# Kernel tuning notes

Hardware: AMD Instinct MI355X
Metric: run time of the kernel (lower is better)

Reference implementation:

```python
import jax, jax.numpy as jnp
import numpy as np

B, S, D, H = 8, 2048, 1024, 128  # batch, seq (== CONTEXT_WINDOW), embed dim, headspace


def setup_inputs() -> dict:
    key = jax.random.key(0)
    ks = jax.random.split(key, 7)
    scale = 1.0 / np.sqrt(D)
    return {
        "x": jax.random.normal(ks[0], (B, S, D), dtype=jnp.float32),
        "Wq": jax.random.normal(ks[1], (D, H), dtype=jnp.float32) * scale,
        "bq": jax.random.normal(ks[2], (H,), dtype=jnp.float32) * 0.01,
        "Wk": jax.random.normal(ks[3], (D, H), dtype=jnp.float32) * scale,
        "bk": jax.random.normal(ks[4], (H,), dtype=jnp.float32) * 0.01,
        "Wv": jax.random.normal(ks[5], (D, H), dtype=jnp.float32) * scale,
        "bv": jax.random.normal(ks[6], (H,), dtype=jnp.float32) * 0.01,
    }


def reference(x, Wq, bq, Wk, bk, Wv, bv):
    # x: [B, S, D]
    embedlen = x.shape[-1]
    q = x @ Wq + bq  # [B, S, H]
    k = x @ Wk + bk  # [B, S, H]
    v = x @ Wv + bv  # [B, S, H]
    # NOTE: original code MULTIPLIES by sqrt(embedlen) (embedlen = full embed dim) --
    # faithful reproduction of the source, not the standard 1/sqrt(head_dim).
    scale = jnp.sqrt(jnp.asarray(embedlen, dtype=x.dtype))
    scores = jnp.einsum("bsh,bth->bst", q, k) * scale  # [B, S, S]
    seqlen = x.shape[1]
    causal = jnp.tril(jnp.ones((seqlen, seqlen), dtype=bool))
    scores = jnp.where(causal, scores, -jnp.inf)
    attn = jax.nn.softmax(scores, axis=-1)
    return jnp.einsum("bst,bth->bsh", attn, v)  # [B, S, H]
```

## Files before the change

### kernel.cpp

```cpp
#include <hip/hip_runtime.h>
#include <math.h>

#define SEQ 2048
#define DIM 1024
#define HD  128
#define NB  8
#define M_TOT (NB * SEQ)

typedef __attribute__((ext_vector_type(8))) short   short8;
typedef __attribute__((ext_vector_type(4))) float   floatx4;

__device__ __forceinline__ unsigned short f2bf(float f) {
    unsigned u = __builtin_bit_cast(unsigned, f);
    u += 0x7FFFu + ((u >> 16) & 1u);
    return (unsigned short)(u >> 16);
}
__device__ __forceinline__ float bf2f(unsigned short h) {
    unsigned u = ((unsigned)h) << 16;
    return __builtin_bit_cast(float, u);
}
__device__ __forceinline__ void async16(const void* g, void* l) {
    __builtin_amdgcn_global_load_lds(
        (const __attribute__((address_space(1))) unsigned int*)g,
        (__attribute__((address_space(3))) unsigned int*)l, 16, 0, 0);
}

#define MFMA16(a, b, c) __builtin_amdgcn_mfma_f32_16x16x32_bf16((a), (b), (c), 0, 0, 0)

__global__ __launch_bounds__(256) void wt_prep(
    const float* __restrict__ Wq, const float* __restrict__ Wk, const float* __restrict__ Wv,
    unsigned short* __restrict__ Wth, unsigned short* __restrict__ Wtl)
{
    int idx = blockIdx.x * 256 + threadIdx.x;
    int k   = idx & 1023;
    int n   = (idx >> 10) & 127;
    int mat = idx >> 17;
    const float* W = (mat == 0) ? Wq : (mat == 1) ? Wk : Wv;
    float v = W[k * HD + n];
    unsigned short hi = f2bf(v);
    Wth[idx] = hi;
    Wtl[idx] = f2bf(v - bf2f(hi));
}

__global__ __launch_bounds__(256) void qkv_gemm(
    const float* __restrict__ x,
    const unsigned short* __restrict__ Wth, const unsigned short* __restrict__ Wtl,
    const float* __restrict__ bq, const float* __restrict__ bk, const float* __restrict__ bv,
    unsigned short* __restrict__ Qh, unsigned short* __restrict__ Ql,
    unsigned short* __restrict__ Kh, unsigned short* __restrict__ Kl,
    unsigned short* __restrict__ Vt)
{
    __shared__ short lds[48 * 512];

    const int t    = threadIdx.x;
    const int lane = t & 63;
    const int w    = t >> 6;
    const int lrow = lane & 15;
    const int quad = lane >> 4;

    const int mat = blockIdx.x;
    const int R0  = blockIdx.y * 64;
    const int mh  = w & 1;
    const int nh  = w >> 1;

    floatx4 acc[2][4];
    const floatx4 zf = {0.f, 0.f, 0.f, 0.f};
    #pragma unroll
    for (int i = 0; i < 2; ++i)
        #pragma unroll
        for (int j = 0; j < 4; ++j) acc[i][j] = zf;

    const size_t wmat = (size_t)mat * (HD * DIM);

    auto stage = [&](int k0, int q) {
        const float* xp = x + (size_t)(R0 + w * 16 + lrow) * DIM + k0 + quad * 8;
        float4 xa = *(const float4*)xp;
        float4 xb = *(const float4*)(xp + 4);
        float xv[8] = {xa.x, xa.y, xa.z, xa.w, xb.x, xb.y, xb.z, xb.w};
        short8 hv, lv;
        #pragma unroll
        for (int i = 0; i < 8; ++i) {
            unsigned short h = f2bf(xv[i]);
            hv[i] = (short)h;
            lv[i] = (short)f2bf(xv[i] - bf2f(h));
        }
        *(short8*)&lds[(q * 24 + w * 2 + 0) * 512 + lane * 8] = hv;
        *(short8*)&lds[(q * 24 + w * 2 + 1) * 512 + lane * 8] = lv;
        #pragma unroll
        for (int i = 0; i < 4; ++i) {
            int id = w * 4 + i;
            int p = id & 1, nf = id >> 1;
            const unsigned short* src = (p ? Wtl : Wth) + wmat
                + (size_t)(nf * 16 + lrow) * DIM + k0 + quad * 8;
            async16(src, &lds[(q * 24 + 8 + id) * 512 + lane * 8]);
        }
    };

    stage(0, 0);
    for (int it = 0; it < 32; ++it) {
        __syncthreads();
        if (it < 31) stage((it + 1) * 32, (it + 1) & 1);
        const int q = it & 1;

        short8 a[2][2];
        #pragma unroll
        for (int mi = 0; mi < 2; ++mi)
            #pragma unroll
            for (int p = 0; p < 2; ++p)
                a[mi][p] = *(short8*)&lds[(q * 24 + (2 * mh + mi) * 2 + p) * 512 + lane * 8];

        #pragma unroll
        for (int ni = 0; ni < 4; ++ni) {
            int nf = nh * 4 + ni;
            short8 bh = *(short8*)&lds[(q * 24 + 8 + nf * 2 + 0) * 512 + lane * 8];
            #pragma unroll
            for (int mi = 0; mi < 2; ++mi)
                acc[mi][ni] = MFMA16(a[mi][0], bh, acc[mi][ni]);
            if (mat < 2) {
                short8 bl = *(short8*)&lds[(q * 24 + 8 + nf * 2 + 1) * 512 + lane * 8];
                #pragma unroll
                for (int mi = 0; mi < 2; ++mi) {
                    acc[mi][ni] = MFMA16(a[mi][0], bl, acc[mi][ni]);
                    acc[mi][ni] = MFMA16(a[mi][1], bh, acc[mi][ni]);
                }
            }
        }
    }

    const float* bias = (mat == 0) ? bq : (mat == 1) ? bk : bv;
    #pragma unroll
    for (int ni = 0; ni < 4; ++ni) {
        int col = (nh * 4 + ni) * 16 + lrow;
        float bval = bias[col];
        #pragma unroll
        for (int mi = 0; mi < 2; ++mi) {
            #pragma unroll
            for (int reg = 0; reg < 4; ++reg) {
                int gm = R0 + (2 * mh + mi) * 16 + quad * 4 + reg;
                float v = acc[mi][ni][reg] + bval;
                if (mat == 0) {
                    v *= 32.0f;
                    unsigned short h = f2bf(v);
                    Qh[(size_t)gm * HD + col] = h;
                    Ql[(size_t)gm * HD + col] = f2bf(v - bf2f(h));
                } else if (mat == 1) {
                    unsigned short h = f2bf(v);
                    Kh[(size_t)gm * HD + col] = h;
                    Kl[(size_t)gm * HD + col] = f2bf(v - bf2f(h));
                } else {
                    int b = gm >> 11, s = gm & 2047;
                    Vt[((size_t)b * HD + col) * SEQ + s] = f2bf(v);
                }
            }
        }
    }
}

__global__ __launch_bounds__(256) void flash_attn(
    const unsigned short* __restrict__ Qh, const unsigned short* __restrict__ Ql,
    const unsigned short* __restrict__ Kh, const unsigned short* __restrict__ Kl,
    const unsigned short* __restrict__ Vt, float* __restrict__ out,
    float* __restrict__ Opart, float* __restrict__ ML, int split)
{
    __shared__ short lds[52 * 512];

    const int t    = threadIdx.x;
    const int lane = t & 63;
    const int w    = t >> 6;
    const int lrow = lane & 15;
    const int quad = lane >> 4;

    const int idx = blockIdx.x;
    const int b   = idx & 7;
    const int h   = split ? ((idx >> 3) & 1) : 0;
    const int s   = split ? (63 - (idx >> 4)) : (63 - (idx >> 3));
    const int T   = (s + 2) >> 1;
    const int Th  = (T + 1) >> 1;
    const int t0  = split ? (h ? Th : 0) : 0;
    const int t1  = split ? (h ? T : Th) : T;

    if (split && t0 >= t1) {
        float* op = Opart + (size_t)idx * 4096;
        for (int i = t; i < 4096; i += 256) op[i] = 0.0f;
        if (t < 32) { ML[(idx * 32 + t) * 2] = -1e30f; ML[(idx * 32 + t) * 2 + 1] = 0.0f; }
        return;
    }

    const int mh = w & 1;
    const int kh = w >> 1;
    const int R  = s * 32 + mh * 16;

    const size_t kbase = (size_t)b * SEQ * HD;
    const size_t vbase = (size_t)b * HD * SEQ;

    short8 qf[4][2];
    #pragma unroll
    for (int kc = 0; kc < 4; ++kc) {
        size_t off = kbase + (size_t)(R + lrow) * HD + kc * 32 + quad * 8;
        qf[kc][0] = *(const short8*)(Qh + off);
        qf[kc][1] = *(const short8*)(Ql + off);
    }

    const floatx4 zf = {0.f, 0.f, 0.f, 0.f};
    floatx4 accO[8];
    #pragma unroll
    for (int i = 0; i < 8; ++i) accO[i] = zf;
    float m_[4] = {-1e30f, -1e30f, -1e30f, -1e30f};
    float l_[4] = {0.f, 0.f, 0.f, 0.f};

    for (int it = t0; it < t1; ++it) {
        const int j0 = it * 64;
        __syncthreads();
        #pragma unroll
        for (int i = 0; i < 12; ++i) {
            int id = w * 12 + i;
            const unsigned short* src;
            if (id < 32) {
                int nt = id >> 3, kc = (id >> 1) & 3, p = id & 1;
                src = (p ? Kl : Kh) + kbase
                    + (size_t)(j0 + nt * 16 + lrow) * HD + kc * 32 + quad * 8;
            } else {
                int v = id - 32, df = v >> 1, kc = v & 1;
                src = Vt + vbase + (size_t)(df * 16 + lrow) * SEQ
                    + j0 + kc * 32 + quad * 8;
            }
            async16(src, &lds[id * 512 + lane * 8]);
        }
        __syncthreads();

        floatx4 S[2] = {zf, zf};
        #pragma unroll
        for (int ntl = 0; ntl < 2; ++ntl) {
            int nt = kh * 2 + ntl;
            #pragma unroll
            for (int kc = 0; kc < 4; ++kc) {
                short8 khf = *(short8*)&lds[(nt * 8 + kc * 2 + 0) * 512 + lane * 8];
                short8 klf = *(short8*)&lds[(nt * 8 + kc * 2 + 1) * 512 + lane * 8];
                S[ntl] = MFMA16(qf[kc][0], khf, S[ntl]);
                S[ntl] = MFMA16(qf[kc][0], klf, S[ntl]);
                S[ntl] = MFMA16(qf[kc][1], khf, S[ntl]);
            }
        }
        if (j0 + kh * 32 + 31 > R) {
            #pragma unroll
            for (int ntl = 0; ntl < 2; ++ntl) {
                int key = j0 + (kh * 2 + ntl) * 16 + lrow;
                #pragma unroll
                for (int reg = 0; reg < 4; ++reg) {
                    if (key > R + quad * 4 + reg) S[ntl][reg] = -INFINITY;
                }
            }
        }
        float alpha[4];
        #pragma unroll
        for (int reg = 0; reg < 4; ++reg) {
            float mx = fmaxf(S[0][reg], S[1][reg]);
            #pragma unroll
            for (int hh = 1; hh < 16; hh <<= 1) mx = fmaxf(mx, __shfl_xor(mx, hh));
            float mnew = fmaxf(fmaxf(m_[reg], mx), -1e30f);
            alpha[reg] = __expf(m_[reg] - mnew);
            m_[reg] = mnew;
            float p0 = __expf(S[0][reg] - mnew);
            float p1 = __expf(S[1][reg] - mnew);
            S[0][reg] = p0; S[1][reg] = p1;
            float ls = p0 + p1;
            #pragma unroll
            for (int hh = 1; hh < 16; hh <<= 1) ls += __shfl_xor(ls, hh);
            l_[reg] = l_[reg] * alpha[reg] + ls;
        }
        #pragma unroll
        for (int i = 0; i < 8; ++i)
            #pragma unroll
            for (int reg = 0; reg < 4; ++reg) accO[i][reg] *= alpha[reg];

        #pragma unroll
        for (int ntl = 0; ntl < 2; ++ntl) {
            #pragma unroll
            for (int reg = 0; reg < 4; ++reg) {
                int kloc = ntl * 16 + lrow;
                int jj = kloc & 7, q2 = (kloc >> 3) & 3;
                int lane2 = (quad * 4 + reg) + (q2 << 4);
                lds[(48 + w) * 512 + lane2 * 8 + jj] = (short)f2bf(S[ntl][reg]);
            }
        }
        short8 pf = *(short8*)&lds[(48 + w) * 512 + lane * 8];
        #pragma unroll
        for (int df = 0; df < 8; ++df) {
            short8 vf = *(short8*)&lds[(32 + df * 2 + kh) * 512 + lane * 8];
            accO[df] = MFMA16(pf, vf, accO[df]);
        }
    }

    __syncthreads();
    float* fl   = (float*)lds;
    float* Obuf = fl;
    float* mlb  = fl + 4096;
    if (lrow == 0) {
        #pragma unroll
        for (int reg = 0; reg < 4; ++reg) {
            int row = quad * 4 + reg;
            mlb[((kh * 2 + mh) * 16 + row) * 2 + 0] = m_[reg];
            mlb[((kh * 2 + mh) * 16 + row) * 2 + 1] = l_[reg];
        }
    }
    __syncthreads();
    float myw[4], Mrow[4], Drow[4];
    #pragma unroll
    for (int reg = 0; reg < 4; ++reg) {
        int row = quad * 4 + reg;
        float mo  = mlb[(((1 - kh) * 2 + mh) * 16 + row) * 2 + 0];
        float lo_ = mlb[(((1 - kh) * 2 + mh) * 16 + row) * 2 + 1];
        float M = fmaxf(m_[reg], mo);
        float d = l_[reg] * __expf(m_[reg] - M) + lo_ * __expf(mo - M);
        Mrow[reg] = M; Drow[reg] = d;
        myw[reg] = split ? __expf(m_[reg] - M) : (__expf(m_[reg] - M) / d);
    }
    if (kh == 0) {
        #pragma unroll
        for (int df = 0; df < 8; ++df)
            #pragma unroll
            for (int reg = 0; reg < 4; ++reg)
                Obuf[(mh * 16 + quad * 4 + reg) * 128 + df * 16 + lrow] =
                    accO[df][reg] * myw[reg];
    }
    __syncthreads();
    if (kh == 1) {
        if (split) {
            float* op = Opart + (size_t)idx * 4096;
            #pragma unroll
            for (int df = 0; df < 8; ++df) {
                #pragma unroll
                for (int reg = 0; reg < 4; ++reg) {
                    int row = mh * 16 + quad * 4 + reg;
                    op[row * 128 + df * 16 + lrow] =
                        Obuf[row * 128 + df * 16 + lrow] + accO[df][reg] * myw[reg];
                }
            }
            if (lrow == 0) {
                #pragma unroll
                for (int reg = 0; reg < 4; ++reg) {
                    int row = mh * 16 + quad * 4 + reg;
                    ML[(idx * 32 + row) * 2 + 0] = Mrow[reg];
                    ML[(idx * 32 + row) * 2 + 1] = Drow[reg];
                }
            }
        } else {
            #pragma unroll
            for (int df = 0; df < 8; ++df) {
                #pragma unroll
                for (int reg = 0; reg < 4; ++reg) {
                    float v = Obuf[(mh * 16 + quad * 4 + reg) * 128 + df * 16 + lrow]
                            + accO[df][reg] * myw[reg];
                    size_t o = ((size_t)(b * SEQ + R + quad * 4 + reg)) * HD + df * 16 + lrow;
                    out[o] = v;
                }
            }
        }
    }
}

__global__ __launch_bounds__(256) void splitk_merge(
    const float* __restrict__ Opart, const float* __restrict__ ML,
    float* __restrict__ out)
{
    int tid = blockIdx.x * 256 + threadIdx.x;
    int row = tid >> 5, c4 = tid & 31;
    int b = row >> 11, r = row & 2047, s = r >> 5, rr = r & 31;
    int i0 = ((63 - s) << 4) + b;
    int i1 = i0 + 8;
    float m0 = ML[(i0 * 32 + rr) * 2], l0 = ML[(i0 * 32 + rr) * 2 + 1];
    float m1 = ML[(i1 * 32 + rr) * 2], l1 = ML[(i1 * 32 + rr) * 2 + 1];
    float M  = fmaxf(m0, m1);
    float w0 = __expf(m0 - M), w1 = __expf(m1 - M);
    float inv = 1.0f / (w0 * l0 + w1 * l1);
    float4 a  = *(const float4*)&Opart[((size_t)i0 * 32 + rr) * 128 + c4 * 4];
    float4 bb = *(const float4*)&Opart[((size_t)i1 * 32 + rr) * 128 + c4 * 4];
    float4 o;
    o.x = (w0 * a.x + w1 * bb.x) * inv;
    o.y = (w0 * a.y + w1 * bb.y) * inv;
    o.z = (w0 * a.z + w1 * bb.z) * inv;
    o.w = (w0 * a.w + w1 * bb.w) * inv;
    *(float4*)&out[(size_t)row * 128 + c4 * 4] = o;
}

extern "C" void kernel_launch(void* const* d_in, const int* in_sizes, int n_in,
                              void* d_out, int out_size, void* d_ws, size_t ws_size,
                              hipStream_t stream) {
    const float* x  = (const float*)d_in[0];
    const float* Wq = (const float*)d_in[1];
    const float* bq = (const float*)d_in[2];
    const float* Wk = (const float*)d_in[3];
    const float* bk = (const float*)d_in[4];
    const float* Wv = (const float*)d_in[5];
    const float* bv = (const float*)d_in[6];
    float* out = (float*)d_out;

    unsigned short* Qh  = (unsigned short*)d_ws;
    unsigned short* Ql  = Qh  + (size_t)M_TOT * HD;
    unsigned short* Kh  = Ql  + (size_t)M_TOT * HD;
    unsigned short* Kl  = Kh  + (size_t)M_TOT * HD;
    unsigned short* Vt  = Kl  + (size_t)M_TOT * HD;
    unsigned short* Wth = Vt  + (size_t)M_TOT * HD;
    unsigned short* Wtl = Wth + (size_t)3 * HD * DIM;
    float* Opart = (float*)(Wtl + (size_t)3 * HD * DIM);
    float* ML    = Opart + (size_t)1024 * 32 * 128;

    const size_t need = 22544384ULL + 16777216ULL + 262144ULL;
    const int split = (ws_size >= need) ? 1 : 0;

    wt_prep<<<(3 * HD * DIM) / 256, 256, 0, stream>>>(Wq, Wk, Wv, Wth, Wtl);
    qkv_gemm<<<dim3(3, 256), 256, 0, stream>>>(x, Wth, Wtl, bq, bk, bv, Qh, Ql, Kh, Kl, Vt);
    flash_attn<<<split ? 1024 : 512, 256, 0, stream>>>(Qh, Ql, Kh, Kl, Vt, out, Opart, ML, split);
    if (split) splitk_merge<<<2048, 256, 0, stream>>>(Opart, ML, out);
}
```

Before: 241.8 us.

## Fuse Q/K/V projections into one GEMM kernel sharing the converted x tile

Replaces the per-matrix QKV GEMM (grid 3x256, 64-row tiles) with a single fused kernel of 512 threads over 32-row tiles that computes Q, K and V together. x is read and split into bf16 hi/lo once instead of three times. The low-part weights are now read straight from global memory into registers rather than staged through LDS. This trades smaller M tiles and more blocks for removing the redundant x loads and conversions, at the risk of lower weight reuse per block and higher register pressure.

```diff
diff --git a/kernel.cpp b/kernel.cpp
--- a/kernel.cpp
+++ b/kernel.cpp
@@ -42,7 +42,7 @@
     Wtl[idx] = f2bf(v - bf2f(hi));
 }
 
-__global__ __launch_bounds__(256) void qkv_gemm(
+__global__ __launch_bounds__(512, 4) void qkv_fused(
     const float* __restrict__ x,
     const unsigned short* __restrict__ Wth, const unsigned short* __restrict__ Wtl,
     const float* __restrict__ bq, const float* __restrict__ bk, const float* __restrict__ bv,
@@ -50,7 +50,7 @@
     unsigned short* __restrict__ Kh, unsigned short* __restrict__ Kl,
     unsigned short* __restrict__ Vt)
 {
-    __shared__ short lds[48 * 512];
+    __shared__ short lds[56 * 512];
 
     const int t    = threadIdx.x;
     const int lane = t & 63;
@@ -58,100 +58,105 @@
     const int lrow = lane & 15;
     const int quad = lane >> 4;
 
-    const int mat = blockIdx.x;
-    const int R0  = blockIdx.y * 64;
-    const int mh  = w & 1;
-    const int nh  = w >> 1;
-
-    floatx4 acc[2][4];
+    const int R0 = blockIdx.x * 32;
+
+    auto stageB = [&](int k0, int qb) {
+        #pragma unroll
+        for (int i = 0; i < 3; ++i) {
+            int bf  = w * 3 + i;
+            int mat = bf >> 3, nf = bf & 7;
+            const unsigned short* src = Wth + (size_t)mat * (HD * DIM)
+                + (size_t)(nf * 16 + lrow) * DIM + k0 + quad * 8;
+            async16(src, &lds[(8 + qb * 24 + bf) * 512 + lane * 8]);
+        }
+    };
+
+    const int arow = t >> 4;
+    const int akk  = (t & 15) * 2;
+    auto xload = [&](int k0) -> float2 {
+        return *(const float2*)&x[(size_t)(R0 + arow) * DIM + k0 + akk];
+    };
+    auto stageA = [&](float2 xv, int qb) {
+        unsigned short h0 = f2bf(xv.x), h1 = f2bf(xv.y);
+        unsigned short l0 = f2bf(xv.x - bf2f(h0)), l1 = f2bf(xv.y - bf2f(h1));
+        int mi = arow >> 4, lr = arow & 15, qd = akk >> 3, el = akk & 7;
+        int base = (qb * 4 + mi * 2) * 512 + (qd * 16 + lr) * 8 + el;
+        short2 hv; hv.x = (short)h0; hv.y = (short)h1;
+        short2 lv; lv.x = (short)l0; lv.y = (short)l1;
+        *(short2*)&lds[base]       = hv;
+        *(short2*)&lds[base + 512] = lv;
+    };
+
+    const unsigned short* bloQ = Wtl + (size_t)(w * 16 + lrow) * DIM + quad * 8;
+    const unsigned short* bloK = bloQ + (size_t)(HD * DIM);
+
+    floatx4 acc[2][3];
     const floatx4 zf = {0.f, 0.f, 0.f, 0.f};
     #pragma unroll
-    for (int i = 0; i < 2; ++i)
-        #pragma unroll
-        for (int j = 0; j < 4; ++j) acc[i][j] = zf;
-
-    const size_t wmat = (size_t)mat * (HD * DIM);
-
-    auto stage = [&](int k0, int q) {
-        const float* xp = x + (size_t)(R0 + w * 16 + lrow) * DIM + k0 + quad * 8;
-        float4 xa = *(const float4*)xp;
-        float4 xb = *(const float4*)(xp + 4);
-        float xv[8] = {xa.x, xa.y, xa.z, xa.w, xb.x, xb.y, xb.z, xb.w};
-        short8 hv, lv;
-        #pragma unroll
-        for (int i = 0; i < 8; ++i) {
-            unsigned short h = f2bf(xv[i]);
-            hv[i] = (short)h;
-            lv[i] = (short)f2bf(xv[i] - bf2f(h));
-        }
-        *(short8*)&lds[(q * 24 + w * 2 + 0) * 512 + lane * 8] = hv;
-        *(short8*)&lds[(q * 24 + w * 2 + 1) * 512 + lane * 8] = lv;
-        #pragma unroll
-        for (int i = 0; i < 4; ++i) {
-            int id = w * 4 + i;
-            int p = id & 1, nf = id >> 1;
-            const unsigned short* src = (p ? Wtl : Wth) + wmat
-                + (size_t)(nf * 16 + lrow) * DIM + k0 + quad * 8;
-            async16(src, &lds[(q * 24 + 8 + id) * 512 + lane * 8]);
-        }
-    };
-
-    stage(0, 0);
+    for (int mi = 0; mi < 2; ++mi)
+        #pragma unroll
+        for (int c = 0; c < 3; ++c) acc[mi][c] = zf;
+
+    float2 xn = xload(0);
+    stageA(xn, 0);
+    stageB(0, 0);
+    xn = xload(32);
+
     for (int it = 0; it < 32; ++it) {
         __syncthreads();
-        if (it < 31) stage((it + 1) * 32, (it + 1) & 1);
-        const int q = it & 1;
+        const int k0 = it * 32;
+        const int q  = it & 1;
+
+        short8 blq = *(const short8*)(bloQ + k0);
+        short8 blk = *(const short8*)(bloK + k0);
+
+        if (it < 31) {
+            stageB(k0 + 32, q ^ 1);
+            stageA(xn, q ^ 1);
+        }
+        if (it < 30) xn = xload(k0 + 64);
 
         short8 a[2][2];
         #pragma unroll
         for (int mi = 0; mi < 2; ++mi)
             #pragma unroll
             for (int p = 0; p < 2; ++p)
-                a[mi][p] = *(short8*)&lds[(q * 24 + (2 * mh + mi) * 2 + p) * 512 + lane * 8];
-
-        #pragma unroll
-        for (int ni = 0; ni < 4; ++ni) {
-            int nf = nh * 4 + ni;
-            short8 bh = *(short8*)&lds[(q * 24 + 8 + nf * 2 + 0) * 512 + lane * 8];
-            #pragma unroll
-            for (int mi = 0; mi < 2; ++mi)
-                acc[mi][ni] = MFMA16(a[mi][0], bh, acc[mi][ni]);
-            if (mat < 2) {
-                short8 bl = *(short8*)&lds[(q * 24 + 8 + nf * 2 + 1) * 512 + lane * 8];
-                #pragma unroll
-                for (int mi = 0; mi < 2; ++mi) {
-                    acc[mi][ni] = MFMA16(a[mi][0], bl, acc[mi][ni]);
-                    acc[mi][ni] = MFMA16(a[mi][1], bh, acc[mi][ni]);
-                }
-            }
-        }
-    }
-
-    const float* bias = (mat == 0) ? bq : (mat == 1) ? bk : bv;
+                a[mi][p] = *(short8*)&lds[(q * 4 + mi * 2 + p) * 512 + lane * 8];
+
+        short8 bhq = *(short8*)&lds[(8 + q * 24 +  0 + w) * 512 + lane * 8];
+        short8 bhk = *(short8*)&lds[(8 + q * 24 +  8 + w) * 512 + lane * 8];
+        short8 bhv = *(short8*)&lds[(8 + q * 24 + 16 + w) * 512 + lane * 8];
+
+        #pragma unroll
+        for (int mi = 0; mi < 2; ++mi) {
+            acc[mi][0] = MFMA16(a[mi][0], bhq, acc[mi][0]);
+            acc[mi][1] = MFMA16(a[mi][0], bhk, acc[mi][1]);
+            acc[mi][2] = MFMA16(a[mi][0], bhv, acc[mi][2]);
+            acc[mi][0] = MFMA16(a[mi][1], bhq, acc[mi][0]);
+            acc[mi][1] = MFMA16(a[mi][1], bhk, acc[mi][1]);
+            acc[mi][0] = MFMA16(a[mi][0], blq, acc[mi][0]);
+            acc[mi][1] = MFMA16(a[mi][0], blk, acc[mi][1]);
+        }
+    }
+
+    const int col = w * 16 + lrow;
+    const float bqv = bq[col], bkv = bk[col], bvv = bv[col];
     #pragma unroll
-    for (int ni = 0; ni < 4; ++ni) {
-        int col = (nh * 4 + ni) * 16 + lrow;
-        float bval = bias[col];
-        #pragma unroll
-        for (int mi = 0; mi < 2; ++mi) {
-            #pragma unroll
-            for (int reg = 0; reg < 4; ++reg) {
-                int gm = R0 + (2 * mh + mi) * 16 + quad * 4 + reg;
-                float v = acc[mi][ni][reg] + bval;
-                if (mat == 0) {
-                    v *= 32.0f;
-                    unsigned short h = f2bf(v);
-                    Qh[(size_t)gm * HD + col] = h;
-                    Ql[(size_t)gm * HD + col] = f2bf(v - bf2f(h));
-                } else if (mat == 1) {
-                    unsigned short h = f2bf(v);
-                    Kh[(size_t)gm * HD + col] = h;
-                    Kl[(size_t)gm * HD + col] = f2bf(v - bf2f(h));
-                } else {
-                    int b = gm >> 11, s = gm & 2047;
-                    Vt[((size_t)b * HD + col) * SEQ + s] = f2bf(v);
-                }
-            }
+    for (int mi = 0; mi < 2; ++mi) {
+        #pragma unroll
+        for (int reg = 0; reg < 4; ++reg) {
+            int gm = R0 + mi * 16 + quad * 4 + reg;
+            float vq = (acc[mi][0][reg] + bqv) * 32.0f;
+            unsigned short h = f2bf(vq);
+            Qh[(size_t)gm * HD + col] = h;
+            Ql[(size_t)gm * HD + col] = f2bf(vq - bf2f(h));
+            float vk = acc[mi][1][reg] + bkv;
+            h = f2bf(vk);
+            Kh[(size_t)gm * HD + col] = h;
+            Kl[(size_t)gm * HD + col] = f2bf(vk - bf2f(h));
+            float vv = acc[mi][2][reg] + bvv;
+            int b = gm >> 11, s = gm & 2047;
+            Vt[((size_t)b * HD + col) * SEQ + s] = f2bf(vv);
         }
     }
 }
@@ -409,7 +414,7 @@
     const int split = (ws_size >= need) ? 1 : 0;
 
     wt_prep<<<(3 * HD * DIM) / 256, 256, 0, stream>>>(Wq, Wk, Wv, Wth, Wtl);
-    qkv_gemm<<<dim3(3, 256), 256, 0, stream>>>(x, Wth, Wtl, bq, bk, bv, Qh, Ql, Kh, Kl, Vt);
+    qkv_fused<<<512, 512, 0, stream>>>(x, Wth, Wtl, bq, bk, bv, Qh, Ql, Kh, Kl, Vt);
     flash_attn<<<split ? 1024 : 512, 256, 0, stream>>>(Qh, Ql, Kh, Kl, Vt, out, Opart, ML, split);
     if (split) splitk_merge<<<2048, 256, 0, stream>>>(Opart, ML, out);
 }
```

After: 250.5 us. +3.6%, slower.
